# Optimization experiments

Measured on AMD Instinct MI355X. Metric: run time of the kernel, lower is better.

Reference implementation:

```python
import jax, jax.numpy as jnp
import numpy as np

N_E = 1024
E_DIM = 64
BETA = 0.4
N_TOK = 131072


def setup_inputs() -> dict:
    key = jax.random.key(0)
    k1, k2 = jax.random.split(key)
    z = jax.random.normal(k1, (N_TOK, E_DIM), dtype=jnp.float32)
    # torch init: uniform(-1/n_e, 1/n_e)
    codebook = jax.random.uniform(k2, (N_E, E_DIM), dtype=jnp.float32,
                                  minval=-1.0 / N_E, maxval=1.0 / N_E)
    return {"z": z, "codebook": codebook}


def reference(z, codebook):
    sg = jax.lax.stop_gradient
    # squared euclidean distances: [N, n_e]
    d = (jnp.sum(z * z, axis=1, keepdims=True)
         + jnp.sum(codebook * codebook, axis=1)
         - 2.0 * jnp.matmul(z, codebook.T))
    idx = jnp.argmin(d, axis=1)                      # [N]
    z_q = codebook[idx]                              # gather, [N, E_DIM]
    # commitment / codebook loss
    vq_loss = (jnp.mean((sg(z_q) - z) ** 2)
               + BETA * jnp.mean((z_q - sg(z)) ** 2))
    # straight-through estimator
    z_q_st = z + sg(z_q - z)
    # codebook usage statistics (mean of one-hot encodings)
    e_mean = jnp.bincount(idx, length=N_E).astype(z.dtype) / jnp.asarray(idx.shape[0], z.dtype)
    usage_loss = -jnp.sum(e_mean * jnp.log(e_mean + 1e-10))
    perplexity = jnp.exp(usage_loss)
    vq_loss = vq_loss + 0.01 * usage_loss
    return z_q_st, vq_loss, idx[:, None], perplexity
```

## Files before the change

### kernel.cpp

```cpp
#include <hip/hip_runtime.h>
#include <math.h>

#define N_TOK 131072
#define N_E   1024
#define E_DIM 64
#define BETA  0.4

#define ZQ_OFF   0
#define LOSS_OFF 8388608
#define IDX_OFF  8388609
#define PERP_OFF 8519681

#define WS_C2    0
#define WS_CNT   4096
#define WS_SSQ   8192
#define WS_WLC   8200
#define WS_FHI   8208
#define WS_FLO   139280
#define WS_WL    270352
#define WS_KEYS  303120
#define WLCAP    8192

typedef short bf16x8 __attribute__((ext_vector_type(8)));
typedef float f32x4  __attribute__((ext_vector_type(4)));
typedef unsigned long long u64;

__device__ __forceinline__ unsigned short f32_to_bf16_rn(float f) {
    unsigned u = __float_as_uint(f);
    unsigned r = (u + 0x7fffu + ((u >> 16) & 1u)) >> 16;
    return (unsigned short)r;
}
__device__ __forceinline__ float bf16_to_f32(unsigned short h) {
    return __uint_as_float(((unsigned)h) << 16);
}
__device__ __forceinline__ void gl2lds16(const void* g, void* l) {
    __builtin_amdgcn_global_load_lds(
        (const __attribute__((address_space(1))) unsigned int*)g,
        (__attribute__((address_space(3))) unsigned int*)l, 16, 0, 0);
}

__global__ void c2_kernel(const float* __restrict__ cb, float* __restrict__ c2,
                          int* __restrict__ counts, int* __restrict__ wlc,
                          double* __restrict__ sum_sq) {
    int e = blockIdx.x * blockDim.x + threadIdx.x;
    if (e < N_E) {
        const float* p = cb + (size_t)e * E_DIM;
        double s = 0.0;
#pragma unroll
        for (int k = 0; k < E_DIM; ++k) {
            double c = (double)p[k];
            s = fma(c, c, s);
        }
        c2[e] = (float)s;
        counts[e] = 0;
        if (e == 0) { *wlc = 0; *sum_sq = 0.0; }
    }
}

__global__ void frag_kernel(const float* __restrict__ cb,
                            unsigned short* __restrict__ fhi,
                            unsigned short* __restrict__ flo,
                            u64* __restrict__ keys) {
    int tid = blockIdx.x * 256 + threadIdx.x;
    if (tid < WLCAP) keys[tid] = ~0ull;
    int j  = tid & 7;
    int l  = (tid >> 3) & 63;
    int cc = tid >> 9;
    int code = (cc >> 1) * 16 + (l & 15);
    int k    = (cc & 1) * 32 + (l >> 4) * 8 + j;
    float f = cb[(size_t)code * E_DIM + k];
    unsigned short h = f32_to_bf16_rn(f);
    unsigned short lo = f32_to_bf16_rn(f - bf16_to_f32(h));
    fhi[tid] = h;
    flo[tid] = lo;
}

__device__ __attribute__((noinline)) int exact_best_serial(
    const float* __restrict__ z, const float* __restrict__ cb,
    const float* __restrict__ c2, int n) {
    const float* zr = z + (size_t)n * E_DIM;
    float r[8];
#pragma unroll
    for (int j = 0; j < 8; ++j) r[j] = __fmul_rn(zr[j], zr[j]);
#pragma unroll 1
    for (int i = 8; i < 64; i += 8)
#pragma unroll
        for (int j = 0; j < 8; ++j)
            r[j] = __fadd_rn(r[j], __fmul_rn(zr[i + j], zr[i + j]));
    float z2 = __fadd_rn(__fadd_rn(__fadd_rn(r[0], r[1]), __fadd_rn(r[2], r[3])),
                         __fadd_rn(__fadd_rn(r[4], r[5]), __fadd_rn(r[6], r[7])));
    u64 bestkey = ~0ull;
#pragma unroll 1
    for (int e = 0; e < N_E; ++e) {
        const float* cp = cb + (size_t)e * E_DIM;
        double m = 0.0;
#pragma unroll 1
        for (int i = 0; i < E_DIM; ++i)
            m = fma((double)zr[i], (double)cp[i], m);
        float d = __fsub_rn(__fadd_rn(z2, c2[e]), __fmul_rn(2.0f, (float)m));
        u64 key = ((u64)__float_as_uint(d) << 32) | (unsigned)e;
        if (key < bestkey) bestkey = key;
    }
    return (int)(bestkey & 0xffffffffu);
}

__global__ __launch_bounds__(256, 4) void vq_main(
    const float* __restrict__ z, const float* __restrict__ cb,
    const float* __restrict__ c2, const unsigned short* __restrict__ fhi_,
    const unsigned short* __restrict__ flo_, int* __restrict__ counts,
    double* __restrict__ sum_sq, int* __restrict__ wl_count,
    int* __restrict__ wl, float margin_u, float* __restrict__ out) {

    __shared__ unsigned char stagebuf[2][16384];
    __shared__ float c2s[N_E];
    __shared__ int   best_s[128];
    __shared__ unsigned char flag_s[128];
    __shared__ double wred[4];

    const int tid  = threadIdx.x;
    const int lane = tid & 63;
    const int wid  = tid >> 6;
    const int col  = lane & 15;
    const int quad = lane >> 4;
    const int blk_tok0 = blockIdx.x * 128;
    const int wave_tok0 = blk_tok0 + wid * 32;

#pragma unroll
    for (int i = 0; i < 4; ++i)
        c2s[tid * 4 + i] = fmaf(-0.5f, c2[tid * 4 + i], 0.25f);

    bf16x8 Ah[2][2], Al[2][2];
#pragma unroll
    for (int m = 0; m < 2; ++m) {
        const float* zr = z + (size_t)(wave_tok0 + m * 16 + col) * E_DIM + quad * 8;
#pragma unroll
        for (int kc = 0; kc < 2; ++kc) {
            float4 u0 = *(const float4*)(zr + kc * 32);
            float4 u1 = *(const float4*)(zr + kc * 32 + 4);
            float f[8] = {u0.x, u0.y, u0.z, u0.w, u1.x, u1.y, u1.z, u1.w};
            union { unsigned short u[8]; bf16x8 v; } h, lo;
#pragma unroll
            for (int j = 0; j < 8; ++j) {
                h.u[j]  = f32_to_bf16_rn(f[j]);
                lo.u[j] = f32_to_bf16_rn(f[j] - bf16_to_f32(h.u[j]));
            }
            Ah[m][kc] = h.v;
            Al[m][kc] = lo.v;
        }
    }

    unsigned k1[2][4], k2[2][4];
#pragma unroll
    for (int m = 0; m < 2; ++m)
#pragma unroll
        for (int r = 0; r < 4; ++r) { k1[m][r] = 0u; k2[m][r] = 0u; }

    const char* hsrc0 = (const char*)fhi_;
    const char* lsrc0 = (const char*)flo_;
    auto stage = [&](int s, int b) {
#pragma unroll
        for (int i = 0; i < 2; ++i) {
            gl2lds16(hsrc0 + s * 8192 + i * 4096 + tid * 16,
                     &stagebuf[b][i * 4096 + wid * 1024]);
            gl2lds16(lsrc0 + s * 8192 + i * 4096 + tid * 16,
                     &stagebuf[b][8192 + i * 4096 + wid * 1024]);
        }
    };

    const f32x4 zero4 = {0.f, 0.f, 0.f, 0.f};
    stage(0, 0);
    for (int s = 0; s < 16; ++s) {
        __syncthreads();
        if (s + 1 < 16) stage(s + 1, (s + 1) & 1);
        const unsigned char* hb = &stagebuf[s & 1][0];
        const unsigned char* lb = &stagebuf[s & 1][8192];
#pragma unroll
        for (int cl = 0; cl < 4; ++cl) {
            const int c = s * 4 + cl;
            const int off0 = (cl * 2) * 1024 + lane * 16;
            union { uint4 u; bf16x8 v; } bh0, bh1, bl0, bl1;
            bh0.u = *(const uint4*)(hb + off0);
            bh1.u = *(const uint4*)(hb + off0 + 1024);
            bl0.u = *(const uint4*)(lb + off0);
            bl1.u = *(const uint4*)(lb + off0 + 1024);
            const float ch = c2s[c * 16 + col];
            const f32x4 cinit = {ch, ch, ch, ch};
            const unsigned ctag = (unsigned)(63 - c);
#pragma unroll
            for (int m = 0; m < 2; ++m) {
                f32x4 acc1 = __builtin_amdgcn_mfma_f32_16x16x32_bf16(Ah[m][0], bh0.v, cinit, 0, 0, 0);
                f32x4 acc2 = __builtin_amdgcn_mfma_f32_16x16x32_bf16(Ah[m][1], bh1.v, zero4, 0, 0, 0);
                acc1 = __builtin_amdgcn_mfma_f32_16x16x32_bf16(Ah[m][0], bl0.v, acc1, 0, 0, 0);
                acc2 = __builtin_amdgcn_mfma_f32_16x16x32_bf16(Ah[m][1], bl1.v, acc2, 0, 0, 0);
                acc1 = __builtin_amdgcn_mfma_f32_16x16x32_bf16(Al[m][0], bh0.v, acc1, 0, 0, 0);
                acc2 = __builtin_amdgcn_mfma_f32_16x16x32_bf16(Al[m][1], bh1.v, acc2, 0, 0, 0);
#pragma unroll
                for (int r = 0; r < 4; ++r) {
                    float u = acc1[r] + acc2[r];
                    unsigned key = (__float_as_uint(u) & 0xFFFFFFC0u) | ctag;
                    unsigned hi2 = min(k1[m][r], key);
                    k2[m][r] = max(k2[m][r], hi2);
                    k1[m][r] = max(k1[m][r], key);
                }
            }
        }
    }

#pragma unroll
    for (int m = 0; m < 2; ++m) {
#pragma unroll
        for (int r = 0; r < 4; ++r) {
            float v1 = __uint_as_float(k1[m][r] & 0xFFFFFFC0u);
            float v2 = __uint_as_float(k2[m][r] & 0xFFFFFFC0u);
            int   b1 = (63 - (int)(k1[m][r] & 63u)) * 16 + col;
#pragma unroll
            for (int d = 1; d < 16; d <<= 1) {
                float o1 = __shfl_xor(v1, d, 64);
                float o2 = __shfl_xor(v2, d, 64);
                int   ob = __shfl_xor(b1, d, 64);
                float n2 = fmaxf(fmaxf(v2, o2), fminf(v1, o1));
                bool take = (o1 > v1) || (o1 == v1 && ob < b1);
                v1 = fmaxf(v1, o1);
                b1 = take ? ob : b1;
                v2 = n2;
            }
            if (col == 0) {
                int tl = wid * 32 + m * 16 + quad * 4 + r;
                int n  = blk_tok0 + tl;
                int best = b1;
                bool fl = (v1 - v2) < margin_u;
                if (fl) {
                    int pos = atomicAdd(wl_count, 1);
                    if (pos < WLCAP) wl[pos] = n;
                    else { best = exact_best_serial(z, cb, c2, n); fl = false; }
                }
                best_s[tl] = best;
                flag_s[tl] = fl ? 1 : 0;
                if (!fl) atomicAdd(&counts[best], 1);
            }
        }
    }
    __syncthreads();

    if (tid < 128) out[IDX_OFF + blk_tok0 + tid] = (float)best_s[tid];

    const int sub = tid & 15, grp = tid >> 4;
    double dl = 0.0;
    const float4* zrow = (const float4*)z;
    const float4* crow = (const float4*)cb;
    float4* qrow = (float4*)(out + ZQ_OFF);
#pragma unroll
    for (int p = 0; p < 8; ++p) {
        int tl = p * 16 + grp;
        if (!flag_s[tl]) {
            int n = blk_tok0 + tl;
            float4 z4 = zrow[(size_t)n * 16 + sub];
            float4 c4 = crow[(size_t)best_s[tl] * 16 + sub];
            float dx = c4.x - z4.x, dy = c4.y - z4.y;
            float dz = c4.z - z4.z, dw = c4.w - z4.w;
            float4 q;
            q.x = z4.x + dx; q.y = z4.y + dy;
            q.z = z4.z + dz; q.w = z4.w + dw;
            qrow[(size_t)n * 16 + sub] = q;
            dl += (double)dx * dx + (double)dy * dy
                + (double)dz * dz + (double)dw * dw;
        }
    }
#pragma unroll
    for (int off = 32; off > 0; off >>= 1)
        dl += __shfl_down(dl, off, 64);
    if (lane == 0) wred[wid] = dl;
    __syncthreads();
    if (tid == 0)
        atomicAdd(sum_sq, wred[0] + wred[1] + wred[2] + wred[3]);
}

__global__ __launch_bounds__(64) void fixup_scan(
    const float* __restrict__ z, const float* __restrict__ cb,
    const float* __restrict__ c2, const int* __restrict__ wl,
    const int* __restrict__ wl_count, u64* __restrict__ keys) {

    int count = *wl_count; if (count > WLCAP) count = WLCAP;
    const int g = blockIdx.x >> 5;
    const int s = blockIdx.x & 31;
    if (g * 64 >= count) return;
    const int lane = threadIdx.x;
    const int w = g * 64 + lane;
    const bool valid = w < count;
    const int n = wl[valid ? w : g * 64];

    double zd[E_DIM];
    const float4* zp = (const float4*)(z + (size_t)n * E_DIM);
#pragma unroll
    for (int k = 0; k < 16; ++k) {
        float4 v = zp[k];
        zd[4 * k]     = (double)v.x;
        zd[4 * k + 1] = (double)v.y;
        zd[4 * k + 2] = (double)v.z;
        zd[4 * k + 3] = (double)v.w;
    }
    float r8[8];
#pragma unroll
    for (int j = 0; j < 8; ++j) {
        float f = (float)zd[j];
        r8[j] = __fmul_rn(f, f);
    }
#pragma unroll
    for (int i = 8; i < 64; i += 8)
#pragma unroll
        for (int j = 0; j < 8; ++j) {
            float f = (float)zd[i + j];
            r8[j] = __fadd_rn(r8[j], __fmul_rn(f, f));
        }
    const float z2 = __fadd_rn(
        __fadd_rn(__fadd_rn(r8[0], r8[1]), __fadd_rn(r8[2], r8[3])),
        __fadd_rn(__fadd_rn(r8[4], r8[5]), __fadd_rn(r8[6], r8[7])));

    u64 best = ~0ull;
    const int e0 = s * 32;
    for (int e = e0; e < e0 + 32; ++e) {
        const float* cp = cb + (size_t)e * E_DIM;
        double m = 0.0;
#pragma unroll
        for (int i = 0; i < E_DIM; ++i)
            m = fma(zd[i], (double)cp[i], m);
        float d = __fsub_rn(__fadd_rn(z2, c2[e]), __fmul_rn(2.0f, (float)m));
        u64 key = ((u64)__float_as_uint(d) << 32) | (unsigned)e;
        if (key < best) best = key;
    }
    if (valid) atomicMin(&keys[w], best);
}

__global__ __launch_bounds__(256) void fixup_apply(
    const float* __restrict__ z, const float* __restrict__ cb,
    const int* __restrict__ wl, const int* __restrict__ wl_count,
    const u64* __restrict__ keys, int* __restrict__ counts,
    double* __restrict__ sum_sq, float* __restrict__ out) {

    int count = *wl_count; if (count > WLCAP) count = WLCAP;
    const int lane = threadIdx.x & 63;
    const int gw = blockIdx.x * 4 + (threadIdx.x >> 6);
    for (int w = gw; w < count; w += 1024) {
        const int n = wl[w];
        const int best = (int)(keys[w] & 0xffffffffull);
        float cv = cb[(size_t)best * E_DIM + lane];
        float zi = z[(size_t)n * E_DIM + lane];
        float diff = cv - zi;
        out[ZQ_OFF + (size_t)n * E_DIM + lane] = zi + diff;
        double d2 = (double)diff * (double)diff;
#pragma unroll
        for (int off = 32; off > 0; off >>= 1)
            d2 += __shfl_down(d2, off, 64);
        if (lane == 0) {
            atomicAdd(sum_sq, d2);
            atomicAdd(&counts[best], 1);
            out[IDX_OFF + n] = (float)best;
        }
    }
}

__global__ __launch_bounds__(1024) void finalize_kernel(
    const int* __restrict__ counts, const double* __restrict__ sum_sq,
    float* __restrict__ out) {
    __shared__ double red[1024];
    int e = threadIdx.x;
    double em = (double)counts[e] / (double)N_TOK;
    red[e] = -em * log(em + 1e-10);
    __syncthreads();
    for (int s = 512; s > 0; s >>= 1) {
        if (e < s) red[e] += red[e + s];
        __syncthreads();
    }
    if (e == 0) {
        double usage = red[0];
        double mse = sum_sq[0] / (double)((size_t)N_TOK * E_DIM);
        out[LOSS_OFF] = (float)((1.0 + BETA) * mse + 0.01 * usage);
        out[PERP_OFF] = (float)exp(usage);
    }
}

extern "C" void kernel_launch(void* const* d_in, const int* in_sizes, int n_in,
                              void* d_out, int out_size, void* d_ws, size_t ws_size,
                              hipStream_t stream) {
    const float* z  = (const float*)d_in[0];
    const float* cb = (const float*)d_in[1];
    float* out = (float*)d_out;

    float*          c2     = (float*)((char*)d_ws + WS_C2);
    int*            counts = (int*)((char*)d_ws + WS_CNT);
    double*         sum_sq = (double*)((char*)d_ws + WS_SSQ);
    int*            wlc    = (int*)((char*)d_ws + WS_WLC);
    unsigned short* fhi    = (unsigned short*)((char*)d_ws + WS_FHI);
    unsigned short* flo    = (unsigned short*)((char*)d_ws + WS_FLO);
    int*            wl     = (int*)((char*)d_ws + WS_WL);
    u64*            keys   = (u64*)((char*)d_ws + WS_KEYS);

    float margin_u = (ws_size >= (size_t)(WS_KEYS + 8 * WLCAP)) ? 2.25e-5f : 0.0f;

    c2_kernel<<<4, 256, 0, stream>>>(cb, c2, counts, wlc, sum_sq);
    frag_kernel<<<256, 256, 0, stream>>>(cb, fhi, flo, keys);
    vq_main<<<1024, 256, 0, stream>>>(z, cb, c2, fhi, flo, counts, sum_sq,
                                      wlc, wl, margin_u, out);
    fixup_scan<<<4096, 64, 0, stream>>>(z, cb, c2, wl, wlc, keys);
    fixup_apply<<<256, 256, 0, stream>>>(z, cb, wl, wlc, keys, counts,
                                         sum_sq, out);
    finalize_kernel<<<1, 1024, 0, stream>>>(counts, sum_sq, out);
}
```

Before: 218.0 us.

## Switch distance screening from split-bf16 MFMA to two-level int8 MFMA

The approximate nearest-code screen changes from bf16 hi/lo MFMA (six per tile) to int8 hi/lo quantization with integer MFMAs (three per tile). Codebook and z are scaled, quantized, and combined into integer keys. The codebook bias is precomputed as scaled integers and the two prep kernels are merged into one. The fixup scan is rebalanced to 256-thread blocks with split FP64 accumulators. This cuts MFMA work and staged LDS bytes, but coarser quantization may flag more ambiguous tokens for the exact fixup path (WLCAP doubled), and an extra barrier is added per stage.

```diff
diff --git a/kernel.cpp b/kernel.cpp
--- a/kernel.cpp
+++ b/kernel.cpp
@@ -12,67 +12,57 @@
 #define PERP_OFF 8519681
 
 #define WS_C2    0
-#define WS_CNT   4096
-#define WS_SSQ   8192
-#define WS_WLC   8200
-#define WS_FHI   8208
-#define WS_FLO   139280
-#define WS_WL    270352
-#define WS_KEYS  303120
-#define WLCAP    8192
-
-typedef short bf16x8 __attribute__((ext_vector_type(8)));
-typedef float f32x4  __attribute__((ext_vector_type(4)));
+#define WS_C2I   4096
+#define WS_CNT   8192
+#define WS_SSQ   12288
+#define WS_WLC   12296
+#define WS_FHI   12304
+#define WS_FLO   77840
+#define WS_WL    143376
+#define WS_KEYS  208912
+#define WLCAP    16384
+
+#define INV_SZ  15.875f
+#define INV_SC  130048.0f
+#define SCALE_D 264257536.0
+#define BIGC    0x20000000
+
+typedef int i32x4 __attribute__((ext_vector_type(4)));
 typedef unsigned long long u64;
 
-__device__ __forceinline__ unsigned short f32_to_bf16_rn(float f) {
-    unsigned u = __float_as_uint(f);
-    unsigned r = (u + 0x7fffu + ((u >> 16) & 1u)) >> 16;
-    return (unsigned short)r;
-}
-__device__ __forceinline__ float bf16_to_f32(unsigned short h) {
-    return __uint_as_float(((unsigned)h) << 16);
-}
 __device__ __forceinline__ void gl2lds16(const void* g, void* l) {
     __builtin_amdgcn_global_load_lds(
         (const __attribute__((address_space(1))) unsigned int*)g,
         (__attribute__((address_space(3))) unsigned int*)l, 16, 0, 0);
 }
 
-__global__ void c2_kernel(const float* __restrict__ cb, float* __restrict__ c2,
-                          int* __restrict__ counts, int* __restrict__ wlc,
-                          double* __restrict__ sum_sq) {
-    int e = blockIdx.x * blockDim.x + threadIdx.x;
-    if (e < N_E) {
-        const float* p = cb + (size_t)e * E_DIM;
+__global__ __launch_bounds__(256) void prep_kernel(
+    const float* __restrict__ cb, float* __restrict__ c2,
+    int* __restrict__ c2i, int* __restrict__ counts, int* __restrict__ wlc,
+    double* __restrict__ sum_sq, char* __restrict__ fhi,
+    char* __restrict__ flo, u64* __restrict__ keys) {
+    int tid = blockIdx.x * 256 + threadIdx.x;
+    int j = tid & 15, l = (tid >> 4) & 63, c = tid >> 10;
+    int code = c * 16 + (l & 15);
+    int k = ((l >> 4) << 4) | j;
+    float cv = cb[code * 64 + k];
+    float f = cv * INV_SC;
+    float h = rintf(f);
+    float lo = rintf((f - h) * 256.f);
+    lo = fminf(fmaxf(lo, -127.f), 127.f);
+    fhi[tid] = (char)(int)h;
+    flo[tid] = (char)(int)lo;
+    if (tid < WLCAP) keys[tid] = ~0ull;
+    if (tid < N_E) {
+        const float* p = cb + tid * 64;
         double s = 0.0;
 #pragma unroll
-        for (int k = 0; k < E_DIM; ++k) {
-            double c = (double)p[k];
-            s = fma(c, c, s);
-        }
-        c2[e] = (float)s;
-        counts[e] = 0;
-        if (e == 0) { *wlc = 0; *sum_sq = 0.0; }
-    }
-}
-
-__global__ void frag_kernel(const float* __restrict__ cb,
-                            unsigned short* __restrict__ fhi,
-                            unsigned short* __restrict__ flo,
-                            u64* __restrict__ keys) {
-    int tid = blockIdx.x * 256 + threadIdx.x;
-    if (tid < WLCAP) keys[tid] = ~0ull;
-    int j  = tid & 7;
-    int l  = (tid >> 3) & 63;
-    int cc = tid >> 9;
-    int code = (cc >> 1) * 16 + (l & 15);
-    int k    = (cc & 1) * 32 + (l >> 4) * 8 + j;
-    float f = cb[(size_t)code * E_DIM + k];
-    unsigned short h = f32_to_bf16_rn(f);
-    unsigned short lo = f32_to_bf16_rn(f - bf16_to_f32(h));
-    fhi[tid] = h;
-    flo[tid] = lo;
+        for (int i = 0; i < 64; ++i) { double d = (double)p[i]; s = fma(d, d, s); }
+        c2[tid] = (float)s;
+        c2i[tid] = (int)llround(s * SCALE_D);
+        counts[tid] = 0;
+    }
+    if (tid == 0) { *wlc = 0; *sum_sq = 0.0; }
 }
 
 __device__ __attribute__((noinline)) int exact_best_serial(
@@ -106,14 +96,15 @@
 
 __global__ __launch_bounds__(256, 4) void vq_main(
     const float* __restrict__ z, const float* __restrict__ cb,
-    const float* __restrict__ c2, const unsigned short* __restrict__ fhi_,
-    const unsigned short* __restrict__ flo_, int* __restrict__ counts,
-    double* __restrict__ sum_sq, int* __restrict__ wl_count,
-    int* __restrict__ wl, float margin_u, float* __restrict__ out) {
-
-    __shared__ unsigned char stagebuf[2][16384];
-    __shared__ float c2s[N_E];
-    __shared__ int   best_s[128];
+    const float* __restrict__ c2, const int* __restrict__ c2i,
+    const char* __restrict__ fhi_, const char* __restrict__ flo_,
+    int* __restrict__ counts, double* __restrict__ sum_sq,
+    int* __restrict__ wl_count, int* __restrict__ wl,
+    unsigned margin_v, float* __restrict__ out) {
+
+    __shared__ char stagebuf[2][8192];
+    __shared__ int  c2i_s[N_E];
+    __shared__ int  best_s[128];
     __shared__ unsigned char flag_s[128];
     __shared__ double wred[4];
 
@@ -126,27 +117,30 @@
     const int wave_tok0 = blk_tok0 + wid * 32;
 
 #pragma unroll
-    for (int i = 0; i < 4; ++i)
-        c2s[tid * 4 + i] = fmaf(-0.5f, c2[tid * 4 + i], 0.25f);
-
-    bf16x8 Ah[2][2], Al[2][2];
+    for (int i = 0; i < 4; ++i) c2i_s[tid * 4 + i] = c2i[tid * 4 + i];
+
+    i32x4 Ah[2], Al[2];
 #pragma unroll
     for (int m = 0; m < 2; ++m) {
-        const float* zr = z + (size_t)(wave_tok0 + m * 16 + col) * E_DIM + quad * 8;
-#pragma unroll
-        for (int kc = 0; kc < 2; ++kc) {
-            float4 u0 = *(const float4*)(zr + kc * 32);
-            float4 u1 = *(const float4*)(zr + kc * 32 + 4);
-            float f[8] = {u0.x, u0.y, u0.z, u0.w, u1.x, u1.y, u1.z, u1.w};
-            union { unsigned short u[8]; bf16x8 v; } h, lo;
-#pragma unroll
-            for (int j = 0; j < 8; ++j) {
-                h.u[j]  = f32_to_bf16_rn(f[j]);
-                lo.u[j] = f32_to_bf16_rn(f[j] - bf16_to_f32(h.u[j]));
-            }
-            Ah[m][kc] = h.v;
-            Al[m][kc] = lo.v;
-        }
+        const float* zr = z + (size_t)(wave_tok0 + m * 16 + col) * E_DIM + quad * 16;
+        float e[16];
+#pragma unroll
+        for (int t = 0; t < 4; ++t) {
+            float4 v = *(const float4*)(zr + t * 4);
+            e[4 * t] = v.x; e[4 * t + 1] = v.y; e[4 * t + 2] = v.z; e[4 * t + 3] = v.w;
+        }
+        union { char b[16]; i32x4 v; } ph, pl;
+#pragma unroll
+        for (int t = 0; t < 16; ++t) {
+            float f = e[t] * INV_SZ;
+            float h = rintf(f);
+            float lo = rintf((f - h) * 256.f);
+            lo = fminf(fmaxf(lo, -127.f), 127.f);
+            ph.b[t] = (char)(int)h;
+            pl.b[t] = (char)(int)lo;
+        }
+        Ah[m] = ph.v;
+        Al[m] = pl.v;
     }
 
     unsigned k1[2][4], k2[2][4];
@@ -155,80 +149,66 @@
 #pragma unroll
         for (int r = 0; r < 4; ++r) { k1[m][r] = 0u; k2[m][r] = 0u; }
 
-    const char* hsrc0 = (const char*)fhi_;
-    const char* lsrc0 = (const char*)flo_;
     auto stage = [&](int s, int b) {
-#pragma unroll
-        for (int i = 0; i < 2; ++i) {
-            gl2lds16(hsrc0 + s * 8192 + i * 4096 + tid * 16,
-                     &stagebuf[b][i * 4096 + wid * 1024]);
-            gl2lds16(lsrc0 + s * 8192 + i * 4096 + tid * 16,
-                     &stagebuf[b][8192 + i * 4096 + wid * 1024]);
-        }
+        gl2lds16(fhi_ + s * 4096 + tid * 16, &stagebuf[b][tid * 16]);
+        gl2lds16(flo_ + s * 4096 + tid * 16, &stagebuf[b][4096 + tid * 16]);
     };
 
-    const f32x4 zero4 = {0.f, 0.f, 0.f, 0.f};
+    const i32x4 zeroi = {0, 0, 0, 0};
     stage(0, 0);
     for (int s = 0; s < 16; ++s) {
         __syncthreads();
         if (s + 1 < 16) stage(s + 1, (s + 1) & 1);
-        const unsigned char* hb = &stagebuf[s & 1][0];
-        const unsigned char* lb = &stagebuf[s & 1][8192];
+        const char* hb = &stagebuf[s & 1][0];
+        const char* lb = &stagebuf[s & 1][4096];
 #pragma unroll
         for (int cl = 0; cl < 4; ++cl) {
             const int c = s * 4 + cl;
-            const int off0 = (cl * 2) * 1024 + lane * 16;
-            union { uint4 u; bf16x8 v; } bh0, bh1, bl0, bl1;
-            bh0.u = *(const uint4*)(hb + off0);
-            bh1.u = *(const uint4*)(hb + off0 + 1024);
-            bl0.u = *(const uint4*)(lb + off0);
-            bl1.u = *(const uint4*)(lb + off0 + 1024);
-            const float ch = c2s[c * 16 + col];
-            const f32x4 cinit = {ch, ch, ch, ch};
+            i32x4 bh = *(const i32x4*)(hb + cl * 1024 + lane * 16);
+            i32x4 bl = *(const i32x4*)(lb + cl * 1024 + lane * 16);
+            int bias = BIGC - c2i_s[c * 16 + col];
+            i32x4 cinit = {bias, bias, bias, bias};
             const unsigned ctag = (unsigned)(63 - c);
 #pragma unroll
             for (int m = 0; m < 2; ++m) {
-                f32x4 acc1 = __builtin_amdgcn_mfma_f32_16x16x32_bf16(Ah[m][0], bh0.v, cinit, 0, 0, 0);
-                f32x4 acc2 = __builtin_amdgcn_mfma_f32_16x16x32_bf16(Ah[m][1], bh1.v, zero4, 0, 0, 0);
-                acc1 = __builtin_amdgcn_mfma_f32_16x16x32_bf16(Ah[m][0], bl0.v, acc1, 0, 0, 0);
-                acc2 = __builtin_amdgcn_mfma_f32_16x16x32_bf16(Ah[m][1], bl1.v, acc2, 0, 0, 0);
-                acc1 = __builtin_amdgcn_mfma_f32_16x16x32_bf16(Al[m][0], bh0.v, acc1, 0, 0, 0);
-                acc2 = __builtin_amdgcn_mfma_f32_16x16x32_bf16(Al[m][1], bh1.v, acc2, 0, 0, 0);
+                i32x4 ahh = __builtin_amdgcn_mfma_i32_16x16x64_i8(Ah[m], bh, zeroi, 0, 0, 0);
+                i32x4 amd = __builtin_amdgcn_mfma_i32_16x16x64_i8(Ah[m], bl, cinit, 0, 0, 0);
+                amd = __builtin_amdgcn_mfma_i32_16x16x64_i8(Al[m], bh, amd, 0, 0, 0);
 #pragma unroll
                 for (int r = 0; r < 4; ++r) {
-                    float u = acc1[r] + acc2[r];
-                    unsigned key = (__float_as_uint(u) & 0xFFFFFFC0u) | ctag;
-                    unsigned hi2 = min(k1[m][r], key);
-                    k2[m][r] = max(k2[m][r], hi2);
+                    unsigned v = ((unsigned)ahh[r] << 8) + (unsigned)amd[r];
+                    unsigned key = (v & 0xFFFFFFC0u) | ctag;
+                    unsigned lo2 = min(k1[m][r], key);
+                    k2[m][r] = max(k2[m][r], lo2);
                     k1[m][r] = max(k1[m][r], key);
                 }
             }
         }
+        __syncthreads();
     }
 
 #pragma unroll
     for (int m = 0; m < 2; ++m) {
 #pragma unroll
         for (int r = 0; r < 4; ++r) {
-            float v1 = __uint_as_float(k1[m][r] & 0xFFFFFFC0u);
-            float v2 = __uint_as_float(k2[m][r] & 0xFFFFFFC0u);
-            int   b1 = (63 - (int)(k1[m][r] & 63u)) * 16 + col;
+            unsigned ku1 = k1[m][r], ku2 = k2[m][r];
+            int b1 = (63 - (int)(ku1 & 63u)) * 16 + col;
 #pragma unroll
             for (int d = 1; d < 16; d <<= 1) {
-                float o1 = __shfl_xor(v1, d, 64);
-                float o2 = __shfl_xor(v2, d, 64);
-                int   ob = __shfl_xor(b1, d, 64);
-                float n2 = fmaxf(fmaxf(v2, o2), fminf(v1, o1));
-                bool take = (o1 > v1) || (o1 == v1 && ob < b1);
-                v1 = fmaxf(v1, o1);
+                unsigned o1 = (unsigned)__shfl_xor((int)ku1, d, 64);
+                unsigned o2 = (unsigned)__shfl_xor((int)ku2, d, 64);
+                int      ob = __shfl_xor(b1, d, 64);
+                unsigned n2 = max(max(ku2, o2), min(ku1, o1));
+                bool take = (o1 > ku1) || (o1 == ku1 && ob < b1);
+                ku1 = max(ku1, o1);
                 b1 = take ? ob : b1;
-                v2 = n2;
+                ku2 = n2;
             }
             if (col == 0) {
                 int tl = wid * 32 + m * 16 + quad * 4 + r;
                 int n  = blk_tok0 + tl;
                 int best = b1;
-                bool fl = (v1 - v2) < margin_u;
+                bool fl = (ku1 - ku2) < margin_v;
                 if (fl) {
                     int pos = atomicAdd(wl_count, 1);
                     if (pos < WLCAP) wl[pos] = n;
@@ -275,16 +255,16 @@
         atomicAdd(sum_sq, wred[0] + wred[1] + wred[2] + wred[3]);
 }
 
-__global__ __launch_bounds__(64) void fixup_scan(
+__global__ __launch_bounds__(256) void fixup_scan(
     const float* __restrict__ z, const float* __restrict__ cb,
     const float* __restrict__ c2, const int* __restrict__ wl,
     const int* __restrict__ wl_count, u64* __restrict__ keys) {
 
     int count = *wl_count; if (count > WLCAP) count = WLCAP;
-    const int g = blockIdx.x >> 5;
-    const int s = blockIdx.x & 31;
+    const int g = blockIdx.x >> 3;
     if (g * 64 >= count) return;
-    const int lane = threadIdx.x;
+    const int lane  = threadIdx.x & 63;
+    const int slice = (blockIdx.x & 7) * 4 + (threadIdx.x >> 6);
     const int w = g * 64 + lane;
     const bool valid = w < count;
     const int n = wl[valid ? w : g * 64];
@@ -317,14 +297,20 @@
         __fadd_rn(__fadd_rn(r8[4], r8[5]), __fadd_rn(r8[6], r8[7])));
 
     u64 best = ~0ull;
-    const int e0 = s * 32;
+    const int e0 = slice * 32;
+#pragma unroll 2
     for (int e = e0; e < e0 + 32; ++e) {
         const float* cp = cb + (size_t)e * E_DIM;
-        double m = 0.0;
-#pragma unroll
-        for (int i = 0; i < E_DIM; ++i)
-            m = fma(zd[i], (double)cp[i], m);
-        float d = __fsub_rn(__fadd_rn(z2, c2[e]), __fmul_rn(2.0f, (float)m));
+        double m0 = 0.0, m1 = 0.0, m2 = 0.0, m3 = 0.0;
+#pragma unroll
+        for (int i = 0; i < 16; ++i) {
+            m0 = fma(zd[i],      (double)cp[i],      m0);
+            m1 = fma(zd[i + 16], (double)cp[i + 16], m1);
+            m2 = fma(zd[i + 32], (double)cp[i + 32], m2);
+            m3 = fma(zd[i + 48], (double)cp[i + 48], m3);
+        }
+        float m32 = (float)((m0 + m1) + (m2 + m3));
+        float d = __fsub_rn(__fadd_rn(z2, c2[e]), __fmul_rn(2.0f, m32));
         u64 key = ((u64)__float_as_uint(d) << 32) | (unsigned)e;
         if (key < best) best = key;
     }
@@ -386,22 +372,24 @@
     const float* cb = (const float*)d_in[1];
     float* out = (float*)d_out;
 
-    float*          c2     = (float*)((char*)d_ws + WS_C2);
-    int*            counts = (int*)((char*)d_ws + WS_CNT);
-    double*         sum_sq = (double*)((char*)d_ws + WS_SSQ);
-    int*            wlc    = (int*)((char*)d_ws + WS_WLC);
-    unsigned short* fhi    = (unsigned short*)((char*)d_ws + WS_FHI);
-    unsigned short* flo    = (unsigned short*)((char*)d_ws + WS_FLO);
-    int*            wl     = (int*)((char*)d_ws + WS_WL);
-    u64*            keys   = (u64*)((char*)d_ws + WS_KEYS);
-
-    float margin_u = (ws_size >= (size_t)(WS_KEYS + 8 * WLCAP)) ? 2.25e-5f : 0.0f;
-
-    c2_kernel<<<4, 256, 0, stream>>>(cb, c2, counts, wlc, sum_sq);
-    frag_kernel<<<256, 256, 0, stream>>>(cb, fhi, flo, keys);
-    vq_main<<<1024, 256, 0, stream>>>(z, cb, c2, fhi, flo, counts, sum_sq,
-                                      wlc, wl, margin_u, out);
-    fixup_scan<<<4096, 64, 0, stream>>>(z, cb, c2, wl, wlc, keys);
+    float*  c2     = (float*)((char*)d_ws + WS_C2);
+    int*    c2i    = (int*)((char*)d_ws + WS_C2I);
+    int*    counts = (int*)((char*)d_ws + WS_CNT);
+    double* sum_sq = (double*)((char*)d_ws + WS_SSQ);
+    int*    wlc    = (int*)((char*)d_ws + WS_WLC);
+    char*   fhi    = (char*)d_ws + WS_FHI;
+    char*   flo    = (char*)d_ws + WS_FLO;
+    int*    wl     = (int*)((char*)d_ws + WS_WL);
+    u64*    keys   = (u64*)((char*)d_ws + WS_KEYS);
+
+    unsigned margin_v =
+        (ws_size >= (size_t)(WS_KEYS + 8 * WLCAP)) ? 26600u : 0u;
+
+    prep_kernel<<<256, 256, 0, stream>>>(cb, c2, c2i, counts, wlc, sum_sq,
+                                         fhi, flo, keys);
+    vq_main<<<1024, 256, 0, stream>>>(z, cb, c2, c2i, fhi, flo, counts,
+                                      sum_sq, wlc, wl, margin_v, out);
+    fixup_scan<<<2048, 256, 0, stream>>>(z, cb, c2, wl, wlc, keys);
     fixup_apply<<<256, 256, 0, stream>>>(z, cb, wl, wlc, keys, counts,
                                          sum_sq, out);
     finalize_kernel<<<1, 1024, 0, stream>>>(counts, sum_sq, out);
```

Result: slower. 298.2 us (+36.8%).
